# Optimization experiments

Measured on AMD Instinct MI355X. Metric: run time of the kernel, lower is better.

## Reference

```python
import jax, jax.numpy as jnp
import numpy as np

EMB = 1024
N_HEAD = 16
HEAD = 64
D_FF = 4 * EMB
LN_EPS = 1e-5


def layernorm(x, g, b):
    mu = jnp.mean(x, axis=-1, keepdims=True)
    var = jnp.mean(jnp.square(x - mu), axis=-1, keepdims=True)
    return (x - mu) * jax.lax.rsqrt(var + LN_EPS) * g + b


def setup_inputs() -> dict:
    key = jax.random.key(0)
    ks = jax.random.split(key, 12)
    s = 0.02
    x = jax.random.normal(ks[0], (4, 2048, EMB), dtype=jnp.float32)
    # per-head Q/K/V projections (no bias), stacked along head axis
    Wq = jax.random.normal(ks[1], (N_HEAD, EMB, HEAD), dtype=jnp.float32) * s
    Wk = jax.random.normal(ks[2], (N_HEAD, EMB, HEAD), dtype=jnp.float32) * s
    Wv = jax.random.normal(ks[3], (N_HEAD, EMB, HEAD), dtype=jnp.float32) * s
    Wo = jax.random.normal(ks[4], (EMB, EMB), dtype=jnp.float32) * s
    bo = jnp.zeros((EMB,), dtype=jnp.float32)
    ln1_g = jnp.ones((EMB,), dtype=jnp.float32)
    ln1_b = jnp.zeros((EMB,), dtype=jnp.float32)
    W1 = jax.random.normal(ks[5], (EMB, D_FF), dtype=jnp.float32) * s
    b1 = jnp.zeros((D_FF,), dtype=jnp.float32)
    W2 = jax.random.normal(ks[6], (D_FF, EMB), dtype=jnp.float32) * s
    b2 = jnp.zeros((EMB,), dtype=jnp.float32)
    ln2_g = jnp.ones((EMB,), dtype=jnp.float32)
    ln2_b = jnp.zeros((EMB,), dtype=jnp.float32)
    return dict(x=x, Wq=Wq, Wk=Wk, Wv=Wv, Wo=Wo, bo=bo, ln1_g=ln1_g,
                ln1_b=ln1_b, W1=W1, b1=b1, W2=W2, b2=b2, ln2_g=ln2_g,
                ln2_b=ln2_b)


def reference(x, Wq, Wk, Wv, Wo, bo, ln1_g, ln1_b, W1, b1, W2, b2, ln2_g, ln2_b):
    B, T, _ = x.shape
    # fused multi-head QKV (equivalent to the per-head Python loop + concat)
    q = jnp.einsum('btd,hdk->bhtk', x, Wq)
    k = jnp.einsum('btd,hdk->bhtk', x, Wk)
    v = jnp.einsum('btd,hdk->bhtk', x, Wv)
    scores = jnp.einsum('bhtk,bhsk->bhts', q, k) / jnp.sqrt(jnp.float32(HEAD))
    att = jax.nn.softmax(scores, axis=-1)
    heads = jnp.einsum('bhts,bhsk->bhtk', att, v)           # [B,H,T,head]
    cat = heads.transpose(0, 2, 1, 3).reshape(B, T, EMB)     # concat over heads
    mha = cat @ Wo + bo
    x = x + layernorm(mha, ln1_g, ln1_b)                     # residual of LN(sublayer)
    ff = jax.nn.gelu(x @ W1 + b1, approximate=False) @ W2 + b2
    x = x + layernorm(ff, ln2_g, ln2_b)
    return x
```

## Files before the change

kernel.cpp:

```cpp
#include <hip/hip_runtime.h>
#include <math.h>


using u16 = unsigned short;
typedef __bf16 bf16x8 __attribute__((ext_vector_type(8)));
typedef __bf16 bf16x4 __attribute__((ext_vector_type(4)));
typedef unsigned short u16x8 __attribute__((ext_vector_type(8)));
typedef unsigned short u16x4 __attribute__((ext_vector_type(4)));
typedef float f32x4 __attribute__((ext_vector_type(4)));

#if defined(__has_builtin)
#if __has_builtin(__builtin_amdgcn_exp2f)
#define EXP2F(x) __builtin_amdgcn_exp2f(x)
#endif
#endif
#ifndef EXP2F
#define EXP2F(x) __expf((x) * 0.69314718055994531f)
#endif

__device__ __forceinline__ float bf2f(u16 h) {
  return __uint_as_float(((unsigned int)h) << 16);
}
__device__ __forceinline__ u16 f2bf(float f) {
  unsigned int u = __float_as_uint(f);
  u += 0x7fffu + ((u >> 16) & 1u);
  return (u16)(u >> 16);
}

__device__ __forceinline__ void gload_lds16(const void* g, void* l) {
  __builtin_amdgcn_global_load_lds(
      (__attribute__((address_space(1))) void*)(g),
      (__attribute__((address_space(3))) void*)(l), 16, 0, 0);
}

__global__ __launch_bounds__(256) void detect_dtype(const u16* __restrict__ x,
                                                    int* __restrict__ flag) {
  __shared__ int cnt[256];
  int c = 0;
#pragma unroll
  for (int j = 0; j < 8; ++j) {
    float v = bf2f(x[threadIdx.x * 8 + j]);
    float a = fabsf(v);
    if (a >= 1e-4f && a <= 64.0f) ++c;
  }
  cnt[threadIdx.x] = c;
  __syncthreads();
  if (threadIdx.x == 0) {
    int t = 0;
    for (int i = 0; i < 256; ++i) t += cnt[i];
    flag[0] = (t < 1638) ? 1 : 0;
  }
}

__global__ __launch_bounds__(256) void cvt_copy(const void* __restrict__ in,
                                                u16* __restrict__ out,
                                                const int* __restrict__ flagp,
                                                long n) {
  long idx = ((long)blockIdx.x * 256 + threadIdx.x) * 4;
  if (idx >= n) return;
  if (*flagp) {
    float4 v = *(const float4*)((const float*)in + idx);
    out[idx] = f2bf(v.x); out[idx + 1] = f2bf(v.y);
    out[idx + 2] = f2bf(v.z); out[idx + 3] = f2bf(v.w);
  } else {
    *(u16x4*)(out + idx) = *(const u16x4*)((const u16*)in + idx);
  }
}

__global__ __launch_bounds__(256) void cvt_vecs(
    const void* s0, const void* s1, const void* s2, const void* s3,
    const void* s4, const void* s5, const void* s6, u16* __restrict__ dst,
    const int* __restrict__ flagp) {
  const int lens[7] = {1024, 1024, 1024, 4096, 1024, 1024, 1024};
  const int offs[7] = {0, 1024, 2048, 3072, 7168, 8192, 9216};
  const void* srcs[7] = {s0, s1, s2, s3, s4, s5, s6};
  int w = blockIdx.x;
  int f = *flagp;
  for (int i = threadIdx.x; i < lens[w]; i += 256)
    dst[offs[w] + i] = f ? f2bf(((const float*)srcs[w])[i])
                         : ((const u16*)srcs[w])[i];
}

__global__ __launch_bounds__(256) void transpose_cvt(
    const void* __restrict__ in, u16* __restrict__ out, int R, int C,
    long inBS, long outBS, const int* __restrict__ flagp) {
  __shared__ u16 tile[32][33];
  int f = *flagp;
  u16* ob = out + (long)blockIdx.z * outBS;
  int c = blockIdx.x * 32 + threadIdx.x;
  int r0 = blockIdx.y * 32;
  if (f) {
    const float* ib = (const float*)in + (long)blockIdx.z * inBS;
#pragma unroll
    for (int i = threadIdx.y; i < 32; i += 8)
      tile[i][threadIdx.x] = f2bf(ib[(long)(r0 + i) * C + c]);
  } else {
    const u16* ib = (const u16*)in + (long)blockIdx.z * inBS;
#pragma unroll
    for (int i = threadIdx.y; i < 32; i += 8)
      tile[i][threadIdx.x] = ib[(long)(r0 + i) * C + c];
  }
  __syncthreads();
  int r = r0 + threadIdx.x;
  int c0 = blockIdx.x * 32;
#pragma unroll
  for (int i = threadIdx.y; i < 32; i += 8)
    ob[(long)(c0 + i) * R + r] = tile[threadIdx.x][i];
}

__global__ __launch_bounds__(256) void kv_frag(const u16* __restrict__ qkv,
                                               u16* __restrict__ KF,
                                               u16* __restrict__ VF) {
  __shared__ u16 Kt[64][72];
  __shared__ u16 Vt[64][72];
  const int jblk = blockIdx.x, bh = blockIdx.y;
  const int b = bh >> 4, h = bh & 15;
  const int tid = threadIdx.x;
  const long j0 = jblk * 64;

  {
    int tt = tid >> 2, c0 = (tid & 3) * 16;
    const u16* src = qkv + (long)(b * 2048 + j0 + tt) * 3072 + h * 64 + c0;
    *(u16x8*)(&Kt[tt][c0]) = *(const u16x8*)(src + 1024);
    *(u16x8*)(&Kt[tt][c0 + 8]) = *(const u16x8*)(src + 1024 + 8);
    *(u16x8*)(&Vt[tt][c0]) = *(const u16x8*)(src + 2048);
    *(u16x8*)(&Vt[tt][c0 + 8]) = *(const u16x8*)(src + 2048 + 8);
  }
  __syncthreads();

  long obase = ((long)bh * 32 + jblk) * 8 * 512;
#pragma unroll
  for (int si = 0; si < 2; ++si) {
    int s = tid * 2 + si;
    int f = s >> 6, ln = s & 63;
    int kt = f >> 2, nt = f & 3;
    int lr = ln & 15, lq = ln >> 4;
    u16x8 ko, vo;
#pragma unroll
    for (int j = 0; j < 8; ++j) {
      ko[j] = Kt[nt * 16 + lr][kt * 32 + lq * 8 + j];
      vo[j] = Vt[kt * 32 + lq * 8 + j][nt * 16 + lr];
    }
    *(u16x8*)(KF + obase + (long)s * 8) = ko;
    *(u16x8*)(VF + obase + (long)s * 8) = vo;
  }
}

__device__ __forceinline__ bf16x8 fragld(const u16* lb, int row, int ks,
                                         int lq) {
  int slot = ((ks << 2) | lq) ^ (row & 7);
  return *(const bf16x8*)(lb + row * 64 + slot * 8);
}

template <int EPI, int BN>
__global__ __launch_bounds__(512, 2) void gemm2ph(
    const u16* __restrict__ A, const u16* __restrict__ Bt,
    const u16* __restrict__ bias, u16* __restrict__ Cout,
    int M, int N, int K) {
  static_assert(BN == 256 || BN == 128, "");
  constexpr int NFQ = BN / 128;
  __shared__ u16 As[2][16384];
  __shared__ u16 Bs[2][BN * 64];
  const int tid = threadIdx.x;
  const int wave = tid >> 6, lane = tid & 63;
  const int lr = lane & 15, lq = lane >> 4;

  const int MT = M >> 8, NTt = N / BN;
  const int nwg = MT * NTt;
  int wg = blockIdx.x;
  if (!(nwg & 7)) wg = (wg & 7) * (nwg >> 3) + (wg >> 3);
  const int tm = wg % MT, tn = wg / MT;
  const long m0 = (long)tm << 8;
  const long n0 = (long)tn * BN;

  const int wm = (wave >> 2) << 7;
  const int wn = (wave & 3) * (BN / 4);

  const int srow = lane >> 3;
  const int skoff = ((lane & 7) ^ srow) * 8;

  auto stage = [&](int buf, int t) {
#pragma unroll
    for (int j = 0; j < 4; ++j)
      gload_lds16(
          A + (m0 + j * 64 + wave * 8 + srow) * (long)K + t * 64 + skoff,
          &As[buf][j * 4096 + (wave << 9)]);
#pragma unroll
    for (int j = 0; j < BN / 64; ++j)
      gload_lds16(
          Bt + (n0 + j * 64 + wave * 8 + srow) * (long)K + t * 64 + skoff,
          &Bs[buf][j * 4096 + (wave << 9)]);
  };

  f32x4 acc[8][2 * NFQ] = {};
  const int NT = K >> 6;
  int cur = 0;

  stage(0, 0);
  __syncthreads();

  for (int t = 0; t < NT; ++t) {
    const u16* Ab = As[cur];
    const u16* Bb = Bs[cur];
    if (t + 1 < NT) stage(cur ^ 1, t + 1);

    bf16x8 a_[4][2], b0_[NFQ][2], b1_[NFQ][2];
#pragma unroll
    for (int mf = 0; mf < 4; ++mf)
#pragma unroll
      for (int ks = 0; ks < 2; ++ks)
        a_[mf][ks] = fragld(Ab, wm + mf * 16 + lr, ks, lq);
#pragma unroll
    for (int nf = 0; nf < NFQ; ++nf)
#pragma unroll
      for (int ks = 0; ks < 2; ++ks)
        b0_[nf][ks] = fragld(Bb, wn + nf * 16 + lr, ks, lq);
#pragma unroll
    for (int mf = 0; mf < 4; ++mf)
#pragma unroll
      for (int nf = 0; nf < NFQ; ++nf)
#pragma unroll
        for (int ks = 0; ks < 2; ++ks)
          acc[mf][nf] = __builtin_amdgcn_mfma_f32_16x16x32_bf16(
              a_[mf][ks], b0_[nf][ks], acc[mf][nf], 0, 0, 0);
#pragma unroll
    for (int nf = 0; nf < NFQ; ++nf)
#pragma unroll
      for (int ks = 0; ks < 2; ++ks)
        b1_[nf][ks] = fragld(Bb, wn + BN / 8 + nf * 16 + lr, ks, lq);
#pragma unroll
    for (int mf = 0; mf < 4; ++mf)
#pragma unroll
      for (int nf = 0; nf < NFQ; ++nf)
#pragma unroll
        for (int ks = 0; ks < 2; ++ks)
          acc[mf][NFQ + nf] = __builtin_amdgcn_mfma_f32_16x16x32_bf16(
              a_[mf][ks], b1_[nf][ks], acc[mf][NFQ + nf], 0, 0, 0);
#pragma unroll
    for (int mf = 0; mf < 4; ++mf)
#pragma unroll
      for (int ks = 0; ks < 2; ++ks)
        a_[mf][ks] = fragld(Ab, wm + 64 + mf * 16 + lr, ks, lq);
#pragma unroll
    for (int mf = 0; mf < 4; ++mf)
#pragma unroll
      for (int nf = 0; nf < NFQ; ++nf)
#pragma unroll
        for (int ks = 0; ks < 2; ++ks)
          acc[4 + mf][NFQ + nf] = __builtin_amdgcn_mfma_f32_16x16x32_bf16(
              a_[mf][ks], b1_[nf][ks], acc[4 + mf][NFQ + nf], 0, 0, 0);
#pragma unroll
    for (int mf = 0; mf < 4; ++mf)
#pragma unroll
      for (int nf = 0; nf < NFQ; ++nf)
#pragma unroll
        for (int ks = 0; ks < 2; ++ks)
          acc[4 + mf][nf] = __builtin_amdgcn_mfma_f32_16x16x32_bf16(
              a_[mf][ks], b0_[nf][ks], acc[4 + mf][nf], 0, 0, 0);

    __syncthreads();
    cur ^= 1;
  }

  const int rq = lq * 4;
#pragma unroll
  for (int mf = 0; mf < 8; ++mf)
#pragma unroll
    for (int nf2 = 0; nf2 < 2 * NFQ; ++nf2) {
      const int col = (int)n0 + wn + nf2 * 16 + lr;
#pragma unroll
      for (int r = 0; r < 4; ++r) {
        const long row = m0 + wm + mf * 16 + rq + r;
        float v = acc[mf][nf2][r];
        if (EPI == 2) {
          v += bf2f(bias[col]);
          v = 0.5f * v * (1.0f + erff(v * 0.70710678118654752f));
        } else if (EPI == 3) {
          v += bf2f(bias[col]);
        }
        Cout[row * (long)N + col] = f2bf(v);
      }
    }
}

__global__ __launch_bounds__(256) void flash_attn(
    const u16* __restrict__ qkv, const u16* __restrict__ KF,
    const u16* __restrict__ VF, u16* __restrict__ cat) {
  const int T = 2048, LD = 3072;
  const float QSCALE = 0.18033688011112042f;
  const float EXPC = 4.3280851226677321f;
  const int bh = blockIdx.y;
  const int b = bh >> 4, h = bh & 15;
  const int tid = threadIdx.x, wave = tid >> 6, lane = tid & 63;
  const int lr = lane & 15, lq = lane >> 4;

  __shared__ u16 Ps[4 * 32 * 72];
  u16* Pw = Ps + wave * 32 * 72;

  const u16* Qb = qkv + (long)(b * 2048) * LD + h * 64;
  const long fbase = (long)bh * 32 * 8 * 512;

  bf16x8 aq[2][2];
#pragma unroll
  for (int st = 0; st < 2; ++st) {
    int qrow = blockIdx.x * 128 + wave * 32 + st * 16 + lr;
#pragma unroll
    for (int kt = 0; kt < 2; ++kt) {
      u16x8 q = *(const u16x8*)(Qb + (long)qrow * LD + kt * 32 + lq * 8);
      bf16x8 t;
#pragma unroll
      for (int j = 0; j < 8; ++j) t[j] = (__bf16)(bf2f(q[j]) * QSCALE);
      aq[st][kt] = t;
    }
  }

  f32x4 o[2][4] = {};
  float lsum[2] = {0.0f, 0.0f};

  for (int jblk = 0; jblk < T / 64; ++jblk) {
    const u16* kf = KF + fbase + (long)jblk * 8 * 512;
    const u16* vf = VF + fbase + (long)jblk * 8 * 512;

    bf16x8 bk[2][4];
#pragma unroll
    for (int kt = 0; kt < 2; ++kt)
#pragma unroll
      for (int nt = 0; nt < 4; ++nt)
        bk[kt][nt] = *(const bf16x8*)(kf + (kt * 4 + nt) * 512 + lane * 8);

    f32x4 s[2][4] = {};
#pragma unroll
    for (int st = 0; st < 2; ++st)
#pragma unroll
      for (int nt = 0; nt < 4; ++nt)
#pragma unroll
        for (int kt = 0; kt < 2; ++kt)
          s[st][nt] = __builtin_amdgcn_mfma_f32_16x16x32_bf16(
              bk[kt][nt], aq[st][kt], s[st][nt], 0, 0, 0);

    bf16x8 bv[2][4];
#pragma unroll
    for (int kt = 0; kt < 2; ++kt)
#pragma unroll
      for (int nt = 0; nt < 4; ++nt)
        bv[kt][nt] = *(const bf16x8*)(vf + (kt * 4 + nt) * 512 + lane * 8);

#pragma unroll
    for (int st = 0; st < 2; ++st)
#pragma unroll
      for (int nt = 0; nt < 4; ++nt) {
        f32x4 p;
#pragma unroll
        for (int r = 0; r < 4; ++r) p[r] = EXP2F(s[st][nt][r] - EXPC);
        lsum[st] += (p[0] + p[1]) + (p[2] + p[3]);
        bf16x4 pk;
#pragma unroll
        for (int r = 0; r < 4; ++r) pk[r] = (__bf16)p[r];
        *(bf16x4*)(Pw + (st * 16 + lr) * 72 + nt * 16 + lq * 4) = pk;
      }

#pragma unroll
    for (int st = 0; st < 2; ++st)
#pragma unroll
      for (int kt = 0; kt < 2; ++kt) {
        bf16x8 ap =
            *(const bf16x8*)(Pw + (st * 16 + lr) * 72 + kt * 32 + lq * 8);
#pragma unroll
        for (int nt = 0; nt < 4; ++nt)
          o[st][nt] = __builtin_amdgcn_mfma_f32_16x16x32_bf16(
              ap, bv[kt][nt], o[st][nt], 0, 0, 0);
      }
  }

#pragma unroll
  for (int st = 0; st < 2; ++st) {
    lsum[st] += __shfl_xor(lsum[st], 16, 64);
    lsum[st] += __shfl_xor(lsum[st], 32, 64);
  }

  u16* ob = cat + (long)(b * 2048) * 1024 + h * 64;
#pragma unroll
  for (int st = 0; st < 2; ++st) {
    int trow = blockIdx.x * 128 + wave * 32 + st * 16 + lq * 4;
#pragma unroll
    for (int r = 0; r < 4; ++r) {
      float linv = 1.0f / __shfl(lsum[st], lq * 4 + r, 64);
#pragma unroll
      for (int nt = 0; nt < 4; ++nt)
        ob[(long)(trow + r) * 1024 + nt * 16 + lr] = f2bf(o[st][nt][r] * linv);
    }
  }
}

__global__ __launch_bounds__(256) void ln_residual(
    const u16* __restrict__ y, const void* __restrict__ res, int res_raw,
    const u16* __restrict__ g, const u16* __restrict__ bb,
    void* __restrict__ out, const int* __restrict__ flagp, int final_out) {
  const long row = blockIdx.x;
  const int tid = threadIdx.x, wave = tid >> 6, lane = tid & 63;
  u16x4 yv = *(const u16x4*)(y + row * 1024 + tid * 4);
  float yy[4];
#pragma unroll
  for (int j = 0; j < 4; ++j) yy[j] = bf2f(yv[j]);
  float s1 = yy[0] + yy[1] + yy[2] + yy[3];
  float s2 = yy[0] * yy[0] + yy[1] * yy[1] + yy[2] * yy[2] + yy[3] * yy[3];
#pragma unroll
  for (int off = 1; off < 64; off <<= 1) {
    s1 += __shfl_xor(s1, off, 64);
    s2 += __shfl_xor(s2, off, 64);
  }
  __shared__ float ws1[4], ws2[4];
  if (lane == 0) { ws1[wave] = s1; ws2[wave] = s2; }
  __syncthreads();
  float t1 = ws1[0] + ws1[1] + ws1[2] + ws1[3];
  float t2 = ws2[0] + ws2[1] + ws2[2] + ws2[3];
  float mu = t1 * (1.0f / 1024.0f);
  float var = t2 * (1.0f / 1024.0f) - mu * mu;
  float rstd = rsqrtf(var + 1e-5f);
  int i = tid * 4;
  bool f32in = res_raw && (*flagp);
  bool f32out = final_out && (*flagp);
#pragma unroll
  for (int j = 0; j < 4; ++j) {
    float rv = f32in ? ((const float*)res)[row * 1024 + i + j]
                     : bf2f(((const u16*)res)[row * 1024 + i + j]);
    float o = rv + (yy[j] - mu) * rstd * bf2f(g[i + j]) + bf2f(bb[i + j]);
    if (f32out)
      ((float*)out)[row * 1024 + i + j] = o;
    else
      ((u16*)out)[row * 1024 + i + j] = f2bf(o);
  }
}

extern "C" void kernel_launch(void* const* d_in, const int* in_sizes, int n_in,
                              void* d_out, int out_size, void* d_ws,
                              size_t ws_size, hipStream_t stream) {
  const void* x_raw = d_in[0];
  const void* Wq = d_in[1];
  const void* Wk = d_in[2];
  const void* Wv = d_in[3];
  const void* Wo = d_in[4];
  const void* bo = d_in[5];
  const void* ln1g = d_in[6];
  const void* ln1b = d_in[7];
  const void* W1 = d_in[8];
  const void* b1 = d_in[9];
  const void* W2 = d_in[10];
  const void* b2 = d_in[11];
  const void* ln2g = d_in[12];
  const void* ln2b = d_in[13];

  char* ws = (char*)d_ws;
  u16* qkv = (u16*)(ws + 0);
  u16* mha = (u16*)(ws + 0);
  u16* h1 = (u16*)(ws + 0);
  u16* cat = (u16*)(ws + 50331648);
  u16* KF = (u16*)(ws + 67108864);
  u16* ff = (u16*)(ws + 67108864);
  u16* xb = (u16*)(ws + 83886080);
  u16* VF = (u16*)(ws + 83886080);
  u16* x1 = (u16*)(ws + 83886080);
  u16* wqkvt = (u16*)(ws + 100663296);
  u16* wot = (u16*)(ws + 106954752);
  u16* w1t = (u16*)(ws + 109051904);
  u16* w2t = (u16*)(ws + 117440512);
  u16* vecs = (u16*)(ws + 125829120);
  int* flag = (int*)(ws + 125853696);

  const u16* v_bo = vecs + 0;
  const u16* v_l1g = vecs + 1024;
  const u16* v_l1b = vecs + 2048;
  const u16* v_b1 = vecs + 3072;
  const u16* v_b2 = vecs + 7168;
  const u16* v_l2g = vecs + 8192;
  const u16* v_l2b = vecs + 9216;

  detect_dtype<<<1, 256, 0, stream>>>((const u16*)x_raw, flag);
  cvt_copy<<<8192, 256, 0, stream>>>(x_raw, xb, flag, 8388608L);
  cvt_vecs<<<7, 256, 0, stream>>>(bo, ln1g, ln1b, b1, b2, ln2g, ln2b, vecs, flag);

  dim3 tb(32, 8);
  transpose_cvt<<<dim3(2, 32, 16), tb, 0, stream>>>(Wq, wqkvt, 1024, 64, 65536, 65536, flag);
  transpose_cvt<<<dim3(2, 32, 16), tb, 0, stream>>>(Wk, wqkvt + 1048576, 1024, 64, 65536, 65536, flag);
  transpose_cvt<<<dim3(2, 32, 16), tb, 0, stream>>>(Wv, wqkvt + 2097152, 1024, 64, 65536, 65536, flag);
  transpose_cvt<<<dim3(32, 32, 1), tb, 0, stream>>>(Wo, wot, 1024, 1024, 0, 0, flag);
  transpose_cvt<<<dim3(128, 32, 1), tb, 0, stream>>>(W1, w1t, 1024, 4096, 0, 0, flag);
  transpose_cvt<<<dim3(32, 128, 1), tb, 0, stream>>>(W2, w2t, 4096, 1024, 0, 0, flag);

  gemm2ph<0, 256><<<384, 512, 0, stream>>>(xb, wqkvt, nullptr, qkv, 8192, 3072, 1024);
  kv_frag<<<dim3(32, 64), 256, 0, stream>>>(qkv, KF, VF);
  flash_attn<<<dim3(16, 64), 256, 0, stream>>>(qkv, KF, VF, cat);
  gemm2ph<3, 128><<<256, 512, 0, stream>>>(cat, wot, v_bo, mha, 8192, 1024, 1024);
  ln_residual<<<8192, 256, 0, stream>>>(mha, x_raw, 1, v_l1g, v_l1b, x1, flag, 0);
  gemm2ph<2, 256><<<512, 512, 0, stream>>>(x1, w1t, v_b1, h1, 8192, 4096, 1024);
  gemm2ph<3, 128><<<256, 512, 0, stream>>>(h1, w2t, v_b2, ff, 8192, 1024, 4096);
  ln_residual<<<8192, 256, 0, stream>>>(ff, x1, 0, v_l2g, v_l2b, d_out, flag, 1);
}
```

Before: 633.8 us.

## Double-buffer K fragments in flash attention, swizzle P in LDS, retile QKV GEMM

The flash attention loop now prefetches the next K block into a second register set while the current block's softmax and PV products run. This is meant to hide global load latency. The P staging buffer drops its padding and uses an XOR swizzle to avoid LDS bank conflicts, and launch_bounds asks for 4 blocks per CU. The QKV GEMM switches to 128-wide tiles with twice as many blocks for better occupancy. The extra register buffer may raise register pressure against the occupancy hint.

```diff
diff --git a/kernel.cpp b/kernel.cpp
--- a/kernel.cpp
+++ b/kernel.cpp
@@ -283,7 +283,7 @@
     }
 }
 
-__global__ __launch_bounds__(256) void flash_attn(
+__global__ __launch_bounds__(256, 4) void flash_attn(
     const u16* __restrict__ qkv, const u16* __restrict__ KF,
     const u16* __restrict__ VF, u16* __restrict__ cat) {
   const int T = 2048, LD = 3072;
@@ -294,11 +294,13 @@
   const int tid = threadIdx.x, wave = tid >> 6, lane = tid & 63;
   const int lr = lane & 15, lq = lane >> 4;
 
-  __shared__ u16 Ps[4 * 32 * 72];
-  u16* Pw = Ps + wave * 32 * 72;
+  __shared__ u16 Ps[4 * 32 * 64];
+  u16* Pw = Ps + wave * 32 * 64;
 
   const u16* Qb = qkv + (long)(b * 2048) * LD + h * 64;
   const long fbase = (long)bh * 32 * 8 * 512;
+  const u16* kf0 = KF + fbase;
+  const u16* vf0 = VF + fbase;
 
   bf16x8 aq[2][2];
 #pragma unroll
@@ -317,16 +319,9 @@
   f32x4 o[2][4] = {};
   float lsum[2] = {0.0f, 0.0f};
 
-  for (int jblk = 0; jblk < T / 64; ++jblk) {
-    const u16* kf = KF + fbase + (long)jblk * 8 * 512;
-    const u16* vf = VF + fbase + (long)jblk * 8 * 512;
-
-    bf16x8 bk[2][4];
-#pragma unroll
-    for (int kt = 0; kt < 2; ++kt)
-#pragma unroll
-      for (int nt = 0; nt < 4; ++nt)
-        bk[kt][nt] = *(const bf16x8*)(kf + (kt * 4 + nt) * 512 + lane * 8);
+  auto proc = [&](bf16x8 (&bk)[2][4], bf16x8 (&bkN)[2][4], int jb, int jn,
+                  bool pf) {
+    const u16* vf = vf0 + (long)jb * 4096;
 
     f32x4 s[2][4] = {};
 #pragma unroll
@@ -346,7 +341,8 @@
         bv[kt][nt] = *(const bf16x8*)(vf + (kt * 4 + nt) * 512 + lane * 8);
 
 #pragma unroll
-    for (int st = 0; st < 2; ++st)
+    for (int st = 0; st < 2; ++st) {
+      const int rr = st * 16 + lr;
 #pragma unroll
       for (int nt = 0; nt < 4; ++nt) {
         f32x4 p;
@@ -356,20 +352,45 @@
         bf16x4 pk;
 #pragma unroll
         for (int r = 0; r < 4; ++r) pk[r] = (__bf16)p[r];
-        *(bf16x4*)(Pw + (st * 16 + lr) * 72 + nt * 16 + lq * 4) = pk;
+        int g = ((nt * 2 + (lq >> 1)) ^ (lr & 7)) * 8 + (lq & 1) * 4;
+        *(bf16x4*)(Pw + rr * 64 + g) = pk;
       }
-
-#pragma unroll
-    for (int st = 0; st < 2; ++st)
+    }
+
+    if (pf) {
+      const u16* kf = kf0 + (long)jn * 4096;
+#pragma unroll
+      for (int kt = 0; kt < 2; ++kt)
+#pragma unroll
+        for (int nt = 0; nt < 4; ++nt)
+          bkN[kt][nt] = *(const bf16x8*)(kf + (kt * 4 + nt) * 512 + lane * 8);
+    }
+
+#pragma unroll
+    for (int st = 0; st < 2; ++st) {
+      const int rr = st * 16 + lr;
 #pragma unroll
       for (int kt = 0; kt < 2; ++kt) {
-        bf16x8 ap =
-            *(const bf16x8*)(Pw + (st * 16 + lr) * 72 + kt * 32 + lq * 8);
+        bf16x8 ap = *(const bf16x8*)(
+            Pw + rr * 64 + (((kt * 4 + lq) ^ (lr & 7)) * 8));
 #pragma unroll
         for (int nt = 0; nt < 4; ++nt)
           o[st][nt] = __builtin_amdgcn_mfma_f32_16x16x32_bf16(
               ap, bv[kt][nt], o[st][nt], 0, 0, 0);
       }
+    }
+  };
+
+  bf16x8 bkA[2][4], bkB[2][4];
+#pragma unroll
+  for (int kt = 0; kt < 2; ++kt)
+#pragma unroll
+    for (int nt = 0; nt < 4; ++nt)
+      bkA[kt][nt] = *(const bf16x8*)(kf0 + (kt * 4 + nt) * 512 + lane * 8);
+
+  for (int j2 = 0; j2 < 16; ++j2) {
+    proc(bkA, bkB, 2 * j2, 2 * j2 + 1, true);
+    proc(bkB, bkA, 2 * j2 + 1, 2 * j2 + 2, j2 < 15);
   }
 
 #pragma unroll
@@ -487,7 +508,7 @@
   transpose_cvt<<<dim3(128, 32, 1), tb, 0, stream>>>(W1, w1t, 1024, 4096, 0, 0, flag);
   transpose_cvt<<<dim3(32, 128, 1), tb, 0, stream>>>(W2, w2t, 4096, 1024, 0, 0, flag);
 
-  gemm2ph<0, 256><<<384, 512, 0, stream>>>(xb, wqkvt, nullptr, qkv, 8192, 3072, 1024);
+  gemm2ph<0, 128><<<768, 512, 0, stream>>>(xb, wqkvt, nullptr, qkv, 8192, 3072, 1024);
   kv_frag<<<dim3(32, 64), 256, 0, stream>>>(qkv, KF, VF);
   flash_attn<<<dim3(16, 64), 256, 0, stream>>>(qkv, KF, VF, cat);
   gemm2ph<3, 128><<<256, 512, 0, stream>>>(cat, wot, v_bo, mha, 8192, 1024, 1024);
```

After: 897.0 us. 1.42x slower.
